# Performance work log

Measured on AMD Instinct MI355X. Metric: run time of the kernel, lower is better.

## Reference

```python
import jax, jax.numpy as jnp
import numpy as np

B, S, H, NH, HD, I, L = 2, 1024, 1024, 16, 64, 4096, 4
EPS = 1e-6


def rmsnorm(x, w):
    # fp32 RMSNorm as in the torch module (inputs already fp32)
    return x * jax.lax.rsqrt(jnp.mean(x * x, axis=-1, keepdims=True) + EPS) * w


def setup_inputs() -> dict:
    key = jax.random.key(0)
    ks = jax.random.split(key, 12)
    s = 0.02  # weight init scale for numerical sanity
    state = jnp.clip(jax.random.normal(ks[1], (B, S, H), jnp.float32), -1.2, 1.2) * 0.4
    return {
        "embedded_inputs": jax.random.normal(ks[0], (B, S, H), jnp.float32),
        "state": state,
        "adapter_w": jax.random.normal(ks[2], (2 * H, H), jnp.float32) * s,
        "norm_w": jnp.ones((L, 4, H), jnp.float32),
        "Wq": jax.random.normal(ks[3], (L, H, H), jnp.float32) * s,
        "Wk": jax.random.normal(ks[4], (L, H, H), jnp.float32) * s,
        "Wv": jax.random.normal(ks[5], (L, H, H), jnp.float32) * s,
        "Wo": jax.random.normal(ks[6], (L, H, H), jnp.float32) * s,
        "W1": jax.random.normal(ks[7], (L, H, 2 * I), jnp.float32) * s,
        "W2": jax.random.normal(ks[8], (L, I, H), jnp.float32) * s,
        "final_norm_w": jnp.ones((H,), jnp.float32),
        "num_iterations": 2,
    }


def _sandwich_block(x, nw, wq, wk, wv, wo, w1, w2, causal):
    b, s_len, h = x.shape
    scale = 1.0 / np.sqrt(HD)
    res = x
    xn = rmsnorm(x, nw[0])
    q = (xn @ wq).reshape(b, s_len, NH, HD)
    k = (xn @ wk).reshape(b, s_len, NH, HD)
    v = (xn @ wv).reshape(b, s_len, NH, HD)
    scores = jnp.einsum('bqhd,bkhd->bhqk', q, k) * scale
    scores = jnp.where(causal, -jnp.inf, scores)
    attn = jax.nn.softmax(scores, axis=-1)
    out = jnp.einsum('bhqk,bkhd->bqhd', attn, v).reshape(b, s_len, h) @ wo
    x = rmsnorm(res + out, nw[1])
    res = x
    xn = rmsnorm(x, nw[2])
    gate, val = jnp.split(xn @ w1, 2, axis=-1)
    x_mlp = (jax.nn.silu(gate) * val) @ w2
    return rmsnorm(res + x_mlp, nw[3])


def reference(embedded_inputs, state, adapter_w, norm_w, Wq, Wk, Wv, Wo, W1, W2, final_norm_w, num_iterations):
    b, s_len, h = embedded_inputs.shape
    causal = jnp.triu(jnp.ones((s_len, s_len), bool), 1)  # True above diagonal -> masked
    for _ in range(int(num_iterations)):
        x = jnp.concatenate([embedded_inputs, state], axis=-1) @ adapter_w
        for l in range(L):
            x = _sandwich_block(x, norm_w[l], Wq[l], Wk[l], Wv[l], Wo[l], W1[l], W2[l], causal)
        state = x
    return rmsnorm(state, final_norm_w)
```

## Files before the change

### kernel.cpp

```cpp
#include <hip/hip_runtime.h>
#include <hip/hip_bf16.h>
#include <math.h>

constexpr int B_  = 2;
constexpr int S_  = 1024;
constexpr int H_  = 1024;
constexpr int NH_ = 16;
constexpr int HD_ = 64;
constexpr int I_  = 4096;
constexpr int L_  = 4;
constexpr int M_  = B_ * S_;
constexpr float EPS_ = 1e-6f;
constexpr int NUM_ITERS_ = 2;
constexpr size_t PSTRIDE_ = (size_t)M_ * H_;

typedef __attribute__((ext_vector_type(8))) short bf16x8;
typedef __attribute__((ext_vector_type(4))) float f32x4;

__device__ __forceinline__ short f2b(float x) {
    return __builtin_bit_cast(short, __float2bfloat16(x));
}
__device__ __forceinline__ float b2f(short s) {
    return __builtin_bit_cast(float, ((unsigned)(unsigned short)s) << 16);
}

__device__ __forceinline__ void lds_load16(void* lds, const void* g) {
    __builtin_amdgcn_global_load_lds(
        (const __attribute__((address_space(1))) void*)g,
        (__attribute__((address_space(3))) void*)lds, 16, 0, 0);
}

__device__ inline float block_reduce_sum(float v) {
    __shared__ float red[8];
    int lane = threadIdx.x & 63, wid = threadIdx.x >> 6;
#pragma unroll
    for (int o = 32; o; o >>= 1) v += __shfl_down(v, o);
    __syncthreads();
    if (lane == 0) red[wid] = v;
    __syncthreads();
    float s = 0.f;
    for (int i = 0; i < 4; ++i) s += red[i];
    return s;
}

__device__ inline float block_reduce_max(float v) {
    __shared__ float red[8];
    int lane = threadIdx.x & 63, wid = threadIdx.x >> 6;
#pragma unroll
    for (int o = 32; o; o >>= 1) v = fmaxf(v, __shfl_down(v, o));
    __syncthreads();
    if (lane == 0) red[wid] = v;
    __syncthreads();
    float s = -INFINITY;
    for (int i = 0; i < 4; ++i) s = fmaxf(s, red[i]);
    return s;
}

template<int BM, int BN, typename OutT>
__global__ __launch_bounds__(256)
void gemm_mfma(const __hip_bfloat16* __restrict__ A,
               const __hip_bfloat16* __restrict__ Bt,
               OutT* __restrict__ C,
               int K, int lda, int ldb, int ldc,
               int NHb, int KS, long sCk,
               long sAb, long sAh, long sBb, long sBh, long sCb, long sCh)
{
    int z  = blockIdx.z;
    int ks = z % KS;
    int zz = z / KS;
    int hb = zz % NHb, bb = zz / NHb;
    A  += bb * sAb + hb * sAh;
    Bt += bb * sBb + hb * sBh;
    C  += bb * sCb + hb * sCh + (long)ks * sCk;

    const int kslice = K / KS;
    const int kbeg = ks * kslice, kend = kbeg + kslice;

    int bm = blockIdx.y * BM, bn = blockIdx.x * BN;

    __shared__ __align__(16) char smemA[BM * 64];
    __shared__ __align__(16) char smemB[BN * 64];

    const int t    = threadIdx.x;
    const int lane = t & 63;
    const int wv   = t >> 6;
    const int lr  = t >> 2;
    const int lsw = ((t & 3) ^ ((lr >> 1) & 3)) * 8;

    constexpr int FM = BM / 32;
    constexpr int FN = BN / 32;
    const int wm = (wv >> 1) * (BM / 2);
    const int wn = (wv & 1) * (BN / 2);
    const int row16 = lane & 15;
    const int kg    = lane >> 4;

    f32x4 acc[FM][FN] = {};

    const char* Ab = (const char*)A;
    const char* Bb = (const char*)Bt;

    for (int k0 = kbeg; k0 < kend; k0 += 32) {
#pragma unroll
        for (int i = 0; i < BM / 64; ++i)
            lds_load16(smemA + i * 4096 + wv * 1024,
                       Ab + (((long)(bm + i * 64 + lr) * lda + k0 + lsw) << 1));
#pragma unroll
        for (int i = 0; i < BN / 64; ++i)
            lds_load16(smemB + i * 4096 + wv * 1024,
                       Bb + (((long)(bn + i * 64 + lr) * ldb + k0 + lsw) << 1));
        __syncthreads();

        bf16x8 af[FM], bfr[FN];
#pragma unroll
        for (int m = 0; m < FM; ++m) {
            int r = wm + m * 16 + row16;
            af[m] = *(const bf16x8*)(smemA + r * 64 + ((kg ^ ((r >> 1) & 3)) << 4));
        }
#pragma unroll
        for (int n = 0; n < FN; ++n) {
            int r = wn + n * 16 + row16;
            bfr[n] = *(const bf16x8*)(smemB + r * 64 + ((kg ^ ((r >> 1) & 3)) << 4));
        }
#pragma unroll
        for (int m = 0; m < FM; ++m)
#pragma unroll
            for (int n = 0; n < FN; ++n)
                acc[m][n] = __builtin_amdgcn_mfma_f32_16x16x32_bf16(
                                af[m], bfr[n], acc[m][n], 0, 0, 0);
        __syncthreads();
    }

#pragma unroll
    for (int m = 0; m < FM; ++m) {
#pragma unroll
        for (int n = 0; n < FN; ++n) {
#pragma unroll
            for (int r = 0; r < 4; ++r) {
                long row = bm + wm + m * 16 + kg * 4 + r;
                long col = bn + wn + n * 16 + row16;
                float val = acc[m][n][r];
                if constexpr (__is_same(OutT, __hip_bfloat16))
                    C[row * ldc + col] = __float2bfloat16(val);
                else
                    C[row * ldc + col] = val;
            }
        }
    }
}

template<int BM, int BN, typename OutT>
static inline void launch_mm(hipStream_t st,
                             const __hip_bfloat16* A, const __hip_bfloat16* Bt, OutT* C,
                             int M, int N, int K, int lda, int ldb, int ldc,
                             int nb = 1, int nh = 1,
                             long sAb = 0, long sAh = 0,
                             long sBb = 0, long sBh = 0,
                             long sCb = 0, long sCh = 0,
                             int ksplit = 1, long sCk = 0)
{
    dim3 grid(N / BN, M / BM, nb * nh * ksplit);
    gemm_mfma<BM, BN, OutT><<<grid, dim3(256), 0, st>>>(
        A, Bt, C, K, lda, ldb, ldc, nh, ksplit, sCk, sAb, sAh, sBb, sBh, sCb, sCh);
}

__global__ __launch_bounds__(256)
void transpose_w(const float* __restrict__ in, __hip_bfloat16* __restrict__ out,
                 int R, int C, long inz, long outz)
{
    in  += blockIdx.z * inz;
    out += blockIdx.z * outz;
    __shared__ float tile[32][33];
    int rb = blockIdx.y * 32, cb = blockIdx.x * 32;
    int tx = threadIdx.x & 31, ty = threadIdx.x >> 5;
#pragma unroll
    for (int i = 0; i < 32; i += 8)
        tile[ty + i][tx] = in[(long)(rb + ty + i) * C + cb + tx];
    __syncthreads();
#pragma unroll
    for (int i = 0; i < 32; i += 8)
        out[(long)(cb + ty + i) * R + rb + tx] = __float2bfloat16(tile[tx][ty + i]);
}

__global__ __launch_bounds__(256)
void transpose_v(const __hip_bfloat16* __restrict__ v, __hip_bfloat16* __restrict__ vT,
                 int ldsrc)
{
    int z = blockIdx.z, b = z >> 4, h = z & 15;
    __shared__ short tile[32][34];
    int sb = blockIdx.x * 32, db = blockIdx.y * 32;
    int tx = threadIdx.x & 31, ty = threadIdx.x >> 5;
    const __hip_bfloat16* src = v + (long)b * S_ * ldsrc + h * 64;
#pragma unroll
    for (int i = 0; i < 32; i += 8)
        tile[ty + i][tx] = __builtin_bit_cast(short, src[(long)(sb + ty + i) * ldsrc + db + tx]);
    __syncthreads();
    __hip_bfloat16* dst = vT + (long)z * 64 * S_;
#pragma unroll
    for (int i = 0; i < 32; i += 8)
        dst[(long)(db + ty + i) * S_ + sb + tx] =
            __builtin_bit_cast(__hip_bfloat16, tile[tx][ty + i]);
}

template<int P, bool WX, typename OutT>
__global__ __launch_bounds__(256)
void rmsnorm_p(const float* __restrict__ xb, const float* __restrict__ parts,
               const float* __restrict__ w, float* __restrict__ xw,
               OutT* __restrict__ out)
{
    long row = blockIdx.x;
    int t = threadIdx.x;
    long idx = row * H_ + t * 4;
    float4 v = {0.f, 0.f, 0.f, 0.f};
    if (xb) v = *(const float4*)&xb[idx];
#pragma unroll
    for (int p = 0; p < P; ++p) {
        float4 pv = *(const float4*)&parts[(size_t)p * PSTRIDE_ + idx];
        v.x += pv.x; v.y += pv.y; v.z += pv.z; v.w += pv.w;
    }
    if constexpr (WX) *(float4*)&xw[idx] = v;
    float ss = v.x * v.x + v.y * v.y + v.z * v.z + v.w * v.w;
    ss = block_reduce_sum(ss);
    float inv = rsqrtf(ss * (1.f / H_) + EPS_);
    float4 wv = *(const float4*)&w[t * 4];
    float4 y = {v.x * inv * wv.x, v.y * inv * wv.y, v.z * inv * wv.z, v.w * inv * wv.w};
    if constexpr (__is_same(OutT, __hip_bfloat16)) {
        short4 o = {f2b(y.x), f2b(y.y), f2b(y.z), f2b(y.w)};
        *(short4*)&out[idx] = o;
    } else {
        *(float4*)&out[idx] = y;
    }
}

template<int P>
__global__ __launch_bounds__(256)
void rmsnorm_dual_p(const float* __restrict__ x, const float* __restrict__ parts,
                    const float* __restrict__ w1, const float* __restrict__ w2,
                    float* __restrict__ xout, __hip_bfloat16* __restrict__ xnout)
{
    long row = blockIdx.x;
    int t = threadIdx.x;
    long idx = row * H_ + t * 4;
    float4 v = *(const float4*)&x[idx];
#pragma unroll
    for (int p = 0; p < P; ++p) {
        float4 pv = *(const float4*)&parts[(size_t)p * PSTRIDE_ + idx];
        v.x += pv.x; v.y += pv.y; v.z += pv.z; v.w += pv.w;
    }
    float ss = v.x * v.x + v.y * v.y + v.z * v.z + v.w * v.w;
    ss = block_reduce_sum(ss);
    float inv = rsqrtf(ss * (1.f / H_) + EPS_);
    float4 w1v = *(const float4*)&w1[t * 4];
    float4 y = {v.x * inv * w1v.x, v.y * inv * w1v.y, v.z * inv * w1v.z, v.w * inv * w1v.w};
    *(float4*)&xout[idx] = y;
    float ss2 = y.x * y.x + y.y * y.y + y.z * y.z + y.w * y.w;
    ss2 = block_reduce_sum(ss2);
    float inv2 = rsqrtf(ss2 * (1.f / H_) + EPS_);
    float4 w2v = *(const float4*)&w2[t * 4];
    short4 o = {f2b(y.x * inv2 * w2v.x), f2b(y.y * inv2 * w2v.y),
                f2b(y.z * inv2 * w2v.z), f2b(y.w * inv2 * w2v.w)};
    *(short4*)&xnout[idx] = o;
}

__global__ __launch_bounds__(256)
void softmax_causal_bf16(__hip_bfloat16* __restrict__ sc, float scale)
{
    long r = blockIdx.x;
    int q = (int)(r % S_);
    __hip_bfloat16* row = sc + r * (long)S_;
    int t = threadIdx.x;
    short4 raw = *(const short4*)&row[t * 4];
    float f[4];
    f[0] = b2f(raw.x) * scale; f[1] = b2f(raw.y) * scale;
    f[2] = b2f(raw.z) * scale; f[3] = b2f(raw.w) * scale;
    float m = -INFINITY;
#pragma unroll
    for (int j = 0; j < 4; ++j)
        if (t * 4 + j <= q) m = fmaxf(m, f[j]);
    m = block_reduce_max(m);
    float e[4], sum = 0.f;
#pragma unroll
    for (int j = 0; j < 4; ++j) {
        e[j] = (t * 4 + j <= q) ? expf(f[j] - m) : 0.f;
        sum += e[j];
    }
    sum = block_reduce_sum(sum);
    float inv = 1.f / sum;
    short4 o = {f2b(e[0] * inv), f2b(e[1] * inv), f2b(e[2] * inv), f2b(e[3] * inv)};
    *(short4*)&row[t * 4] = o;
}

__global__ __launch_bounds__(256)
void concat_bf16(const float* __restrict__ E, const float* __restrict__ st,
                 __hip_bfloat16* __restrict__ cat)
{
    long n4 = (long)M_ * 2 * H_ / 4;
    for (long i = (long)blockIdx.x * blockDim.x + threadIdx.x; i < n4;
         i += (long)gridDim.x * blockDim.x) {
        long m = i / (2 * H_ / 4);
        long c4 = i % (2 * H_ / 4);
        const float* src = (c4 < H_ / 4) ? &E[m * H_ + c4 * 4]
                                         : &st[m * H_ + (c4 * 4 - H_)];
        float4 v = *(const float4*)src;
        short4 o = {f2b(v.x), f2b(v.y), f2b(v.z), f2b(v.w)};
        *(short4*)&cat[i * 4] = o;
    }
}

__global__ __launch_bounds__(256)
void silu_gate(const __hip_bfloat16* __restrict__ h, __hip_bfloat16* __restrict__ g)
{
    long n4 = (long)M_ * I_ / 4;
    for (long i = (long)blockIdx.x * blockDim.x + threadIdx.x; i < n4;
         i += (long)gridDim.x * blockDim.x) {
        long m = i / (I_ / 4);
        long c = (i % (I_ / 4)) * 4;
        short4 gt = *(const short4*)&h[m * (2 * I_) + c];
        short4 vl = *(const short4*)&h[m * (2 * I_) + I_ + c];
        float gx = b2f(gt.x), gy = b2f(gt.y), gz = b2f(gt.z), gw = b2f(gt.w);
        float y0 = gx / (1.f + expf(-gx)) * b2f(vl.x);
        float y1 = gy / (1.f + expf(-gy)) * b2f(vl.y);
        float y2 = gz / (1.f + expf(-gz)) * b2f(vl.z);
        float y3 = gw / (1.f + expf(-gw)) * b2f(vl.w);
        short4 o = {f2b(y0), f2b(y1), f2b(y2), f2b(y3)};
        *(short4*)&g[m * I_ + c] = o;
    }
}

extern "C" void kernel_launch(void* const* d_in, const int* in_sizes, int n_in,
                              void* d_out, int out_size, void* d_ws, size_t ws_size,
                              hipStream_t stream)
{
    const float* E   = (const float*)d_in[0];
    const float* st0 = (const float*)d_in[1];
    const float* Wa  = (const float*)d_in[2];
    const float* NW  = (const float*)d_in[3];
    const float* Wq  = (const float*)d_in[4];
    const float* Wk  = (const float*)d_in[5];
    const float* Wv  = (const float*)d_in[6];
    const float* Wo  = (const float*)d_in[7];
    const float* W1  = (const float*)d_in[8];
    const float* W2  = (const float*)d_in[9];
    const float* FNW = (const float*)d_in[10];
    float* out = (float*)d_out;
    (void)in_sizes; (void)n_in; (void)out_size;

    typedef __hip_bfloat16 bf16;

    const size_t RESIDENT_BYTES = 266000000;
    const bool resident = ws_size >= RESIDENT_BYTES;

    char* base = (char*)d_ws;
    size_t off = 0;
    auto alloc = [&](size_t bytes) -> char* {
        char* p = base + off;
        off += (bytes + 255) & ~(size_t)255;
        return p;
    };
    bf16* WaT   = (bf16*)alloc((size_t)H_ * 2 * H_ * 2);
    bf16* WqkvT = (bf16*)alloc((size_t)L_ * 3 * H_ * H_ * 2);
    bf16* WoT   = (bf16*)alloc((size_t)L_ * H_ * H_ * 2);
    bf16* W1T   = (bf16*)alloc((resident ? (size_t)L_ : 1) * 2 * I_ * H_ * 2);
    bf16* W2T   = (bf16*)alloc((resident ? (size_t)L_ : 1) * H_ * I_ * 2);
    bf16*  cat  = (bf16*)alloc((size_t)M_ * 2 * H_ * 2);
    float* x    = (float*)alloc((size_t)M_ * H_ * 4);
    bf16*  xn   = (bf16*)alloc((size_t)M_ * H_ * 2);
    bf16*  qkv  = (bf16*)alloc((size_t)M_ * 3 * H_ * 2);
    bf16*  vT   = (bf16*)alloc((size_t)M_ * H_ * 2);
    bf16*  ob   = (bf16*)alloc((size_t)M_ * H_ * 2);
    char*  scores_raw = alloc((size_t)B_ * NH_ * S_ * S_ * 2);
    bf16*  scores = (bf16*)scores_raw;
    bf16*  hbuf   = (bf16*)scores_raw;
    float* parts  = (float*)scores_raw;
    bf16*  gbuf   = (bf16*)alloc((size_t)M_ * I_ * 2);

    transpose_w<<<dim3(H_ / 32, 2 * H_ / 32, 1), 256, 0, stream>>>(
        Wa, WaT, 2 * H_, H_, 0, 0);
    transpose_w<<<dim3(H_ / 32, H_ / 32, L_), 256, 0, stream>>>(
        Wq, WqkvT + 0 * H_ * H_, H_, H_, (long)H_ * H_, (long)3 * H_ * H_);
    transpose_w<<<dim3(H_ / 32, H_ / 32, L_), 256, 0, stream>>>(
        Wk, WqkvT + 1 * H_ * H_, H_, H_, (long)H_ * H_, (long)3 * H_ * H_);
    transpose_w<<<dim3(H_ / 32, H_ / 32, L_), 256, 0, stream>>>(
        Wv, WqkvT + 2 * H_ * H_, H_, H_, (long)H_ * H_, (long)3 * H_ * H_);
    transpose_w<<<dim3(H_ / 32, H_ / 32, L_), 256, 0, stream>>>(
        Wo, WoT, H_, H_, (long)H_ * H_, (long)H_ * H_);
    if (resident) {
        transpose_w<<<dim3(2 * I_ / 32, H_ / 32, L_), 256, 0, stream>>>(
            W1, W1T, H_, 2 * I_, (long)H_ * 2 * I_, (long)H_ * 2 * I_);
        transpose_w<<<dim3(H_ / 32, I_ / 32, L_), 256, 0, stream>>>(
            W2, W2T, I_, H_, (long)I_ * H_, (long)I_ * H_);
    }

    const float scale = 0.125f;
    const float* state = st0;

    for (int it = 0; it < NUM_ITERS_; ++it) {
        concat_bf16<<<dim3(4096), 256, 0, stream>>>(E, state, cat);
        launch_mm<128, 128, float>(stream, cat, WaT, parts,
                                   M_, H_, 2 * H_, 2 * H_, 2 * H_, H_,
                                   1, 1, 0, 0, 0, 0, 0, 0,
                                   4, (long)PSTRIDE_);

        for (int l = 0; l < L_; ++l) {
            const float* nw   = NW + (size_t)l * 4 * H_;
            const bf16* wqkvT = WqkvT + (size_t)l * 3 * H_ * H_;
            const bf16* woT   = WoT + (size_t)l * H_ * H_;
            const bf16* w1T;
            const bf16* w2T;
            if (resident) {
                w1T = W1T + (size_t)l * 2 * I_ * H_;
                w2T = W2T + (size_t)l * H_ * I_;
            } else {
                transpose_w<<<dim3(2 * I_ / 32, H_ / 32, 1), 256, 0, stream>>>(
                    W1 + (size_t)l * H_ * 2 * I_, W1T, H_, 2 * I_, 0, 0);
                transpose_w<<<dim3(H_ / 32, I_ / 32, 1), 256, 0, stream>>>(
                    W2 + (size_t)l * I_ * H_, W2T, I_, H_, 0, 0);
                w1T = W1T;
                w2T = W2T;
            }

            if (l == 0)
                rmsnorm_p<4, true, bf16><<<M_, 256, 0, stream>>>(
                    nullptr, parts, nw + 0 * H_, x, xn);
            else
                rmsnorm_p<0, false, bf16><<<M_, 256, 0, stream>>>(
                    x, nullptr, nw + 0 * H_, nullptr, xn);

            launch_mm<128, 128, bf16>(stream, xn, wqkvT, qkv,
                                      M_, 3 * H_, H_, H_, H_, 3 * H_);

            launch_mm<128, 128, bf16>(stream, qkv, qkv + H_, scores,
                                      S_, S_, HD_, 3 * H_, 3 * H_, S_,
                                      B_, NH_,
                                      (long)S_ * 3 * H_, 64,
                                      (long)S_ * 3 * H_, 64,
                                      (long)NH_ * S_ * S_, (long)S_ * S_);

            softmax_causal_bf16<<<B_ * NH_ * S_, 256, 0, stream>>>(scores, scale);

            transpose_v<<<dim3(S_ / 32, 2, B_ * NH_), 256, 0, stream>>>(
                qkv + 2 * H_, vT, 3 * H_);

            launch_mm<128, 64, bf16>(stream, scores, vT, ob,
                                     S_, 64, S_, S_, S_, H_,
                                     B_, NH_,
                                     (long)NH_ * S_ * S_, (long)S_ * S_,
                                     (long)NH_ * 64 * S_, (long)64 * S_,
                                     (long)S_ * H_, 64);

            launch_mm<128, 128, float>(stream, ob, woT, parts,
                                       M_, H_, H_, H_, H_, H_,
                                       1, 1, 0, 0, 0, 0, 0, 0,
                                       4, (long)PSTRIDE_);

            rmsnorm_dual_p<4><<<M_, 256, 0, stream>>>(
                x, parts, nw + 1 * H_, nw + 2 * H_, x, xn);

            launch_mm<128, 128, bf16>(stream, xn, w1T, hbuf,
                                      M_, 2 * I_, H_, H_, H_, 2 * I_);

            silu_gate<<<dim3(8192), 256, 0, stream>>>(hbuf, gbuf);

            launch_mm<128, 128, float>(stream, gbuf, w2T, parts,
                                       M_, H_, I_, I_, I_, H_,
                                       1, 1, 0, 0, 0, 0, 0, 0,
                                       4, (long)PSTRIDE_);

            rmsnorm_p<4, false, float><<<M_, 256, 0, stream>>>(
                x, parts, nw + 3 * H_, nullptr, x);
        }
        state = x;
    }

    rmsnorm_p<0, false, float><<<M_, 256, 0, stream>>>(
        x, nullptr, FNW, nullptr, out);
}
```

Measured before the change: 2.325 ms.

## Replace materialized attention scores with a fused causal flash-attention kernel

Replaces the QK^T GEMM, the full-row softmax kernel and the PV GEMM with one flash-attention kernel that uses an online softmax, skips key tiles above the causal diagonal, and keeps scores in registers and LDS. This removes writing and re-reading the B*NH*S*S bf16 score matrix and about half of the masked work. The grid has only 8x32 blocks with uneven causal work per block, which may limit occupancy and load balance. Probabilities are rounded to bf16 before the PV MFMA, as in the old path.

```diff
diff --git a/kernel.cpp b/kernel.cpp
--- a/kernel.cpp
+++ b/kernel.cpp
@@ -43,19 +43,6 @@
     return s;
 }
 
-__device__ inline float block_reduce_max(float v) {
-    __shared__ float red[8];
-    int lane = threadIdx.x & 63, wid = threadIdx.x >> 6;
-#pragma unroll
-    for (int o = 32; o; o >>= 1) v = fmaxf(v, __shfl_down(v, o));
-    __syncthreads();
-    if (lane == 0) red[wid] = v;
-    __syncthreads();
-    float s = -INFINITY;
-    for (int i = 0; i < 4; ++i) s = fmaxf(s, red[i]);
-    return s;
-}
-
 template<int BM, int BN, typename OutT>
 __global__ __launch_bounds__(256)
 void gemm_mfma(const __hip_bfloat16* __restrict__ A,
@@ -161,6 +148,191 @@
     dim3 grid(N / BN, M / BM, nb * nh * ksplit);
     gemm_mfma<BM, BN, OutT><<<grid, dim3(256), 0, st>>>(
         A, Bt, C, K, lda, ldb, ldc, nh, ksplit, sCk, sAb, sAh, sBb, sBh, sCb, sCh);
+}
+
+__global__ __launch_bounds__(256)
+void flash_attn(const __hip_bfloat16* __restrict__ qkv,
+                const __hip_bfloat16* __restrict__ vT,
+                __hip_bfloat16* __restrict__ ob, float scale)
+{
+    constexpr int KB = 128;
+    const int qt = blockIdx.x;
+    const int z  = blockIdx.y;
+    const int b  = z >> 4, h = z & 15;
+
+    __shared__ __align__(16) char sK[KB * 128];
+    __shared__ __align__(16) char sV[64 * 256];
+    __shared__ __align__(16) char sP[4][32 * 256];
+
+    const int t    = threadIdx.x;
+    const int lane = t & 63;
+    const int wv   = t >> 6;
+    const int l15  = lane & 15;
+    const int kg   = lane >> 4;
+
+    const long qbase = (long)b * S_ * 3 * H_;
+    const int wq0 = qt * 128 + wv * 32;
+
+    bf16x8 qf[2][2];
+#pragma unroll
+    for (int qb = 0; qb < 2; ++qb)
+#pragma unroll
+        for (int ks = 0; ks < 2; ++ks)
+            qf[qb][ks] = *(const bf16x8*)&qkv[qbase +
+                (long)(wq0 + qb * 16 + l15) * (3 * H_) + h * 64 + ks * 32 + kg * 8];
+
+    f32x4 oacc[2][4] = {};
+    float mrow[2][4], lrow[2][4];
+#pragma unroll
+    for (int qb = 0; qb < 2; ++qb)
+#pragma unroll
+        for (int r = 0; r < 4; ++r) { mrow[qb][r] = -INFINITY; lrow[qb][r] = 0.f; }
+
+    const int ntiles = qt + 1;
+    for (int tile = 0; tile < ntiles; ++tile) {
+        const int kv0 = tile * KB;
+        __syncthreads();
+#pragma unroll
+        for (int rnd = 0; rnd < 4; ++rnd) {
+            int row = rnd * 32 + (t >> 3);
+            int cb  = ((t & 7) * 16) ^ ((row & 7) << 4);
+            lds_load16(sK + rnd * 4096 + wv * 1024,
+                       (const char*)qkv +
+                       ((qbase + (long)(kv0 + row) * (3 * H_) + H_ + h * 64) << 1) + cb);
+        }
+#pragma unroll
+        for (int rnd = 0; rnd < 4; ++rnd) {
+            int row = rnd * 16 + (t >> 4);
+            int cb  = ((t & 15) * 16) ^ ((row & 7) << 4);
+            lds_load16(sV + rnd * 4096 + wv * 1024,
+                       (const char*)vT + (((long)(z * 64 + row) * S_ + kv0) << 1) + cb);
+        }
+        __syncthreads();
+
+        if (kv0 > wq0 + 31) continue;
+
+        f32x4 s[2][8] = {};
+#pragma unroll
+        for (int cb = 0; cb < 8; ++cb) {
+#pragma unroll
+            for (int ks = 0; ks < 2; ++ks) {
+                int krow = cb * 16 + l15;
+                bf16x8 kf = *(const bf16x8*)(sK + krow * 128 +
+                                             ((ks * 64 + kg * 16) ^ ((krow & 7) << 4)));
+#pragma unroll
+                for (int qb = 0; qb < 2; ++qb)
+                    s[qb][cb] = __builtin_amdgcn_mfma_f32_16x16x32_bf16(
+                                    qf[qb][ks], kf, s[qb][cb], 0, 0, 0);
+            }
+        }
+
+        float tmax[2][4];
+#pragma unroll
+        for (int qb = 0; qb < 2; ++qb)
+#pragma unroll
+            for (int r = 0; r < 4; ++r) tmax[qb][r] = -INFINITY;
+#pragma unroll
+        for (int qb = 0; qb < 2; ++qb) {
+#pragma unroll
+            for (int cb = 0; cb < 8; ++cb) {
+#pragma unroll
+                for (int r = 0; r < 4; ++r) {
+                    float v = s[qb][cb][r] * scale;
+                    int kq = kv0 + cb * 16 + l15;
+                    int qq = wq0 + qb * 16 + kg * 4 + r;
+                    v = (kq <= qq) ? v : -INFINITY;
+                    s[qb][cb][r] = v;
+                    tmax[qb][r] = fmaxf(tmax[qb][r], v);
+                }
+            }
+        }
+#pragma unroll
+        for (int qb = 0; qb < 2; ++qb)
+#pragma unroll
+            for (int r = 0; r < 4; ++r) {
+                float v = tmax[qb][r];
+                v = fmaxf(v, __shfl_xor(v, 1));
+                v = fmaxf(v, __shfl_xor(v, 2));
+                v = fmaxf(v, __shfl_xor(v, 4));
+                v = fmaxf(v, __shfl_xor(v, 8));
+                tmax[qb][r] = v;
+            }
+
+        float tsum[2][4];
+#pragma unroll
+        for (int qb = 0; qb < 2; ++qb) {
+#pragma unroll
+            for (int r = 0; r < 4; ++r) {
+                float mn = fmaxf(mrow[qb][r], tmax[qb][r]);
+                float c  = __expf(mrow[qb][r] - mn);
+                mrow[qb][r] = mn;
+                lrow[qb][r] *= c;
+                tsum[qb][r] = 0.f;
+#pragma unroll
+                for (int db = 0; db < 4; ++db) oacc[qb][db][r] *= c;
+            }
+        }
+#pragma unroll
+        for (int qb = 0; qb < 2; ++qb) {
+#pragma unroll
+            for (int cb = 0; cb < 8; ++cb) {
+#pragma unroll
+                for (int r = 0; r < 4; ++r) {
+                    float p = __expf(s[qb][cb][r] - mrow[qb][r]);
+                    tsum[qb][r] += p;
+                    int qloc = qb * 16 + kg * 4 + r;
+                    int kvb  = (cb * 16 + l15) * 2;
+                    *(short*)(sP[wv] + qloc * 256 + (kvb ^ ((qloc & 7) << 4))) = f2b(p);
+                }
+            }
+        }
+#pragma unroll
+        for (int qb = 0; qb < 2; ++qb)
+#pragma unroll
+            for (int r = 0; r < 4; ++r) {
+                float v = tsum[qb][r];
+                v += __shfl_xor(v, 1);
+                v += __shfl_xor(v, 2);
+                v += __shfl_xor(v, 4);
+                v += __shfl_xor(v, 8);
+                lrow[qb][r] += v;
+            }
+
+#pragma unroll
+        for (int ks2 = 0; ks2 < 4; ++ks2) {
+            bf16x8 pf[2];
+#pragma unroll
+            for (int qb = 0; qb < 2; ++qb) {
+                int qloc = qb * 16 + l15;
+                pf[qb] = *(const bf16x8*)(sP[wv] + qloc * 256 +
+                                          ((ks2 * 64 + kg * 16) ^ ((qloc & 7) << 4)));
+            }
+#pragma unroll
+            for (int db = 0; db < 4; ++db) {
+                int drow = db * 16 + l15;
+                bf16x8 vf = *(const bf16x8*)(sV + drow * 256 +
+                                             ((ks2 * 64 + kg * 16) ^ ((drow & 7) << 4)));
+#pragma unroll
+                for (int qb = 0; qb < 2; ++qb)
+                    oacc[qb][db] = __builtin_amdgcn_mfma_f32_16x16x32_bf16(
+                                       pf[qb], vf, oacc[qb][db], 0, 0, 0);
+            }
+        }
+    }
+
+#pragma unroll
+    for (int qb = 0; qb < 2; ++qb) {
+#pragma unroll
+        for (int r = 0; r < 4; ++r) {
+            float inv = 1.f / lrow[qb][r];
+            long row = (long)b * S_ + wq0 + qb * 16 + kg * 4 + r;
+#pragma unroll
+            for (int db = 0; db < 4; ++db) {
+                long col = h * 64 + db * 16 + l15;
+                ob[row * H_ + col] = __float2bfloat16(oacc[qb][db][r] * inv);
+            }
+        }
+    }
 }
 
 __global__ __launch_bounds__(256)
@@ -259,34 +431,6 @@
     short4 o = {f2b(y.x * inv2 * w2v.x), f2b(y.y * inv2 * w2v.y),
                 f2b(y.z * inv2 * w2v.z), f2b(y.w * inv2 * w2v.w)};
     *(short4*)&xnout[idx] = o;
-}
-
-__global__ __launch_bounds__(256)
-void softmax_causal_bf16(__hip_bfloat16* __restrict__ sc, float scale)
-{
-    long r = blockIdx.x;
-    int q = (int)(r % S_);
-    __hip_bfloat16* row = sc + r * (long)S_;
-    int t = threadIdx.x;
-    short4 raw = *(const short4*)&row[t * 4];
-    float f[4];
-    f[0] = b2f(raw.x) * scale; f[1] = b2f(raw.y) * scale;
-    f[2] = b2f(raw.z) * scale; f[3] = b2f(raw.w) * scale;
-    float m = -INFINITY;
-#pragma unroll
-    for (int j = 0; j < 4; ++j)
-        if (t * 4 + j <= q) m = fmaxf(m, f[j]);
-    m = block_reduce_max(m);
-    float e[4], sum = 0.f;
-#pragma unroll
-    for (int j = 0; j < 4; ++j) {
-        e[j] = (t * 4 + j <= q) ? expf(f[j] - m) : 0.f;
-        sum += e[j];
-    }
-    sum = block_reduce_sum(sum);
-    float inv = 1.f / sum;
-    short4 o = {f2b(e[0] * inv), f2b(e[1] * inv), f2b(e[2] * inv), f2b(e[3] * inv)};
-    *(short4*)&row[t * 4] = o;
 }
 
 __global__ __launch_bounds__(256)
@@ -367,10 +511,10 @@
     bf16*  qkv  = (bf16*)alloc((size_t)M_ * 3 * H_ * 2);
     bf16*  vT   = (bf16*)alloc((size_t)M_ * H_ * 2);
     bf16*  ob   = (bf16*)alloc((size_t)M_ * H_ * 2);
-    char*  scores_raw = alloc((size_t)B_ * NH_ * S_ * S_ * 2);
-    bf16*  scores = (bf16*)scores_raw;
-    bf16*  hbuf   = (bf16*)scores_raw;
-    float* parts  = (float*)scores_raw;
+    char*  big  = alloc((size_t)M_ * 2 * I_ * 4 > (size_t)4 * PSTRIDE_ * 4
+                        ? (size_t)M_ * 2 * I_ * 4 : (size_t)4 * PSTRIDE_ * 4);
+    bf16*  hbuf   = (bf16*)big;
+    float* parts  = (float*)big;
     bf16*  gbuf   = (bf16*)alloc((size_t)M_ * I_ * 2);
 
     transpose_w<<<dim3(H_ / 32, 2 * H_ / 32, 1), 256, 0, stream>>>(
@@ -428,24 +572,11 @@
             launch_mm<128, 128, bf16>(stream, xn, wqkvT, qkv,
                                       M_, 3 * H_, H_, H_, H_, 3 * H_);
 
-            launch_mm<128, 128, bf16>(stream, qkv, qkv + H_, scores,
-                                      S_, S_, HD_, 3 * H_, 3 * H_, S_,
-                                      B_, NH_,
-                                      (long)S_ * 3 * H_, 64,
-                                      (long)S_ * 3 * H_, 64,
-                                      (long)NH_ * S_ * S_, (long)S_ * S_);
-
-            softmax_causal_bf16<<<B_ * NH_ * S_, 256, 0, stream>>>(scores, scale);
-
             transpose_v<<<dim3(S_ / 32, 2, B_ * NH_), 256, 0, stream>>>(
                 qkv + 2 * H_, vT, 3 * H_);
 
-            launch_mm<128, 64, bf16>(stream, scores, vT, ob,
-                                     S_, 64, S_, S_, S_, H_,
-                                     B_, NH_,
-                                     (long)NH_ * S_ * S_, (long)S_ * S_,
-                                     (long)NH_ * 64 * S_, (long)64 * S_,
-                                     (long)S_ * H_, 64);
+            flash_attn<<<dim3(S_ / 128, B_ * NH_), 256, 0, stream>>>(
+                qkv, vT, ob, scale);
 
             launch_mm<128, 128, float>(stream, ob, woT, parts,
                                        M_, H_, H_, H_, H_, H_,
```

After: 1.998 ms. 1.16x faster.
